# Kernel tuning notes

Measured on AMD Instinct MI355X. Metric: run time of the kernel, lower is better.

Reference implementation:

```python
import jax, jax.numpy as jnp
import numpy as np

IMG = 224      # img_size
P = 16         # patch_size
C = 3          # in_chans
K = 100        # n_segments
COMPACT = 10.0 # slic compactness
ITERS = 10     # slic k-means iterations


def _resize_matrix(src, dst):
    # Linear antialiased resize is a linear map; materialize it by resizing identity.
    return jax.image.resize(jnp.eye(src, dtype=jnp.float32), (dst, src),
                            method='linear', antialias=True)


def _slic_labels(img_hwc):
    """Simplified SLIC: grid-initialized k-means in (color, compactness-scaled xy) space."""
    H, W = IMG, IMG
    S = float(np.sqrt(H * W / K))         # superpixel spacing
    ratio = COMPACT / S                   # spatial scaling (SLIC distance weighting)
    yy, xx = jnp.meshgrid(jnp.arange(H, dtype=jnp.float32),
                          jnp.arange(W, dtype=jnp.float32), indexing='ij')
    feat = jnp.concatenate([img_hwc, (yy * ratio)[..., None], (xx * ratio)[..., None]],
                           axis=-1).reshape(H * W, C + 2)  # [HW, 5]
    # grid init of K centers
    gh = int(np.ceil(np.sqrt(K)))
    gw = int(np.ceil(K / gh))
    cy = ((np.arange(gh) + 0.5) * H / gh).astype(np.int32)
    cx = ((np.arange(gw) + 0.5) * W / gw).astype(np.int32)
    idx = (cy[:, None] * W + cx[None, :]).reshape(-1)[:K]
    centers0 = feat[jnp.asarray(idx)]  # [K, 5]

    f2 = jnp.sum(feat * feat, axis=1, keepdims=True)  # [HW,1]

    def dists(centers):
        c2 = jnp.sum(centers * centers, axis=1)  # [K]
        return f2 + c2[None, :] - 2.0 * (feat @ centers.T)  # [HW,K]

    def body(i, centers):
        lbl = jnp.argmin(dists(centers), axis=1)              # [HW]
        oh = jax.nn.one_hot(lbl, K, dtype=feat.dtype)         # [HW,K]
        cnt = oh.sum(0)                                       # [K]
        new = (oh.T @ feat) / jnp.maximum(cnt, 1.0)[:, None]  # [K,5]
        return jnp.where((cnt > 0)[:, None], new, centers)

    centers = jax.lax.fori_loop(0, ITERS, body, centers0)
    return jnp.argmin(dists(centers), axis=1).reshape(H, W)


def _embed_one(img_chw, A):
    img = jnp.transpose(img_chw, (1, 2, 0))                     # [H,W,C]
    labels = jax.lax.stop_gradient(_slic_labels(img))           # [H,W] int
    masks = jax.nn.one_hot(labels, K, dtype=img.dtype, axis=0)  # [K,H,W]
    masked = masks[..., None] * img[None]                       # [K,H,W,C]
    tmp = jnp.einsum('ph,khwc->kpwc', A, masked)                # resize rows
    return jnp.einsum('qw,kpwc->kpqc', A, tmp)                  # [K,P,P,C]


def reference(x):
    B = x.shape[0]
    A = _resize_matrix(IMG, P)
    sp = jax.vmap(lambda im: _embed_one(im, A))(x)  # [B,K,P,P,C]
    # torch: view(B, K*C, P, P)  (raw row-major reinterpret), flatten(2), transpose(1,2)
    out = sp.reshape(B, K * C, P, P).reshape(B, K * C, P * P)
    return jnp.transpose(out, (0, 2, 1))  # [B, P*P, K*C]


def setup_inputs() -> dict:
    key = jax.random.key(0)
    x = jax.random.uniform(key, (8, C, IMG, IMG), dtype=jnp.float32)
    return {"x": x}
```

## Files before the change

kernel.cpp:

```cpp
#include <hip/hip_runtime.h>
#include <math.h>

#define IMGD 224
#define HW 50176
#define NK 100
#define NB 8
#define OUT_PER_B 76800
#define NCHUNK 131
#define MSTR 13


static __device__ __forceinline__ float ratio_f32() {
  return (float)(10.0 / sqrt(224.0 * 224.0 / 100.0));
}

static __device__ __forceinline__ float dist5s(float f0, float f1, float f2,
                                               float f3, float f4, float fsq,
                                               float c0, float c1, float c2,
                                               float c3, float c4, float q) {
  float dot = __fmul_rn(f0, c0);
  dot = __fmaf_rn(f1, c1, dot);
  dot = __fmaf_rn(f2, c2, dot);
  dot = __fmaf_rn(f3, c3, dot);
  dot = __fmaf_rn(f4, c4, dot);
  return __fsub_rn(__fadd_rn(fsq, q), __fmul_rn(2.0f, dot));
}

static __device__ __forceinline__ float fsq5(float f0, float f1, float f2,
                                             float f3, float f4) {
  float s = __fmul_rn(f0, f0);
  s = __fadd_rn(s, __fmul_rn(f1, f1));
  s = __fadd_rn(s, __fmul_rn(f2, f2));
  s = __fadd_rn(s, __fmul_rn(f3, f3));
  s = __fadd_rn(s, __fmul_rn(f4, f4));
  return s;
}

__global__ void __launch_bounds__(128, 4) iter_kernel(
    const float* __restrict__ x, float* __restrict__ centers,
    const float* __restrict__ c2g, float* __restrict__ partials, int flag,
    float* __restrict__ Ag) {
  __shared__ float4 ck4[NK];
  __shared__ float2 ck2[NK];
  __shared__ unsigned int mask[NK * MSTR];
  __shared__ unsigned short ppk[NK * MSTR];
  __shared__ float4 cval4[384];
  __shared__ float  cvalf[384];
  __shared__ int cnt[128];
  __shared__ int offx[128];
  __shared__ int wtot;
  __shared__ float ubpart[12][10];
  __shared__ float ubg[12];
  __shared__ unsigned int candm[12][4];
  __shared__ unsigned char clist[12][104];
  __shared__ int clen[12];
  __shared__ float ared[128];
  int c = blockIdx.x, b = blockIdx.y;
  int tid = threadIdx.x;

  if (c >= NCHUNK) {
    for (int rr = 0; rr < 2; ++rr) {
      int p = 2 * b + rr;
      float cp = (p + 0.5f) * 14.0f - 0.5f;
      float trip0, trip1 = 0.0f;
      {
        float xd = fabsf(cp - (float)tid) / 14.0f;
        trip0 = fmaxf(0.0f, 1.0f - xd);
      }
      int t2 = tid + 128;
      if (t2 < IMGD) {
        float xd = fabsf(cp - (float)t2) / 14.0f;
        trip1 = fmaxf(0.0f, 1.0f - xd);
      }
      ared[tid] = trip0 + trip1;
      __syncthreads();
      for (int s = 64; s > 0; s >>= 1) {
        if (tid < s) ared[tid] += ared[tid + s];
        __syncthreads();
      }
      float Zp = ared[0];
      __syncthreads();
      {
        float xd = fabsf(cp - (float)tid) / 14.0f;
        Ag[p * IMGD + tid] = fmaxf(0.0f, 1.0f - xd) / Zp;
      }
      if (t2 < IMGD) {
        float xd = fabsf(cp - (float)t2) / 14.0f;
        Ag[p * IMGD + t2] = fmaxf(0.0f, 1.0f - xd) / Zp;
      }
      __syncthreads();
    }
    return;
  }

  int start = (c < 129) ? c * 384 : 49536 + (c - 129) * 320;
  int len   = (c < 129) ? 384 : 320;

  const float ratio = ratio_f32();
  const float* x0 = x + (size_t)b * 3 * HW;
  if (flag == 0) {
    if (tid < NK) {
      int gy = tid / 10, gx = tid - 10 * (tid / 10);
      int cy = (int)((gy + 0.5) * 224.0 / 10.0);
      int cx = (int)((gx + 0.5) * 224.0 / 10.0);
      int i = cy * IMGD + cx;
      float c0 = x0[i], c1 = x0[HW + i], c2 = x0[2 * HW + i];
      float c3 = __fmul_rn((float)cy, ratio);
      float c4 = __fmul_rn((float)cx, ratio);
      float s = __fmul_rn(c0, c0);
      s = __fadd_rn(s, __fmul_rn(c1, c1));
      s = __fadd_rn(s, __fmul_rn(c2, c2));
      s = __fadd_rn(s, __fmul_rn(c3, c3));
      s = __fadd_rn(s, __fmul_rn(c4, c4));
      ck4[tid] = make_float4(c0, c1, c2, c3);
      ck2[tid] = make_float2(c4, s);
      if (c == 0) {
        float* oc = centers + ((size_t)b * NK + tid) * 5;
        oc[0] = c0; oc[1] = c1; oc[2] = c2; oc[3] = c3; oc[4] = c4;
      }
    }
  } else {
    const float* cb = centers + (size_t)b * NK * 5;
    const float* c2b = c2g + (size_t)b * NK;
    if (tid < NK) {
      ck4[tid] = make_float4(cb[tid*5+0], cb[tid*5+1], cb[tid*5+2], cb[tid*5+3]);
      ck2[tid] = make_float2(cb[tid*5+4], c2b[tid]);
    }
  }
  for (int t = tid; t < NK * MSTR; t += 128) mask[t] = 0u;
  if (tid < 48) candm[tid >> 2][tid & 3] = 0u;

  float f0[3], f1[3], f2[3], f3[3], f4[3], fq[3];
  bool vld[3];
  for (int r = 0; r < 3; ++r) {
    int t = tid + r * 128;
    vld[r] = (t < len);
    int i = start + (vld[r] ? t : 0);
    int y = i / IMGD, xw = i - y * IMGD;
    f0[r] = x0[i]; f1[r] = x0[HW + i]; f2[r] = x0[2 * HW + i];
    f3[r] = __fmul_rn((float)y, ratio);
    f4[r] = __fmul_rn((float)xw, ratio);
    fq[r] = fsq5(f0[r], f1[r], f2[r], f3[r], f4[r]);
  }
  __syncthreads();

  if (tid < 120) {
    int g = tid / 10, kb = tid - 10 * g;
    int i0 = start + g * 32, i1 = i0 + 31;
    int ymin = i0 / IMGD, ymax = i1 / IMGD;
    int cmin = (ymin == ymax) ? (i0 - ymin * IMGD) : 0;
    int cmax = (ymin == ymax) ? (i1 - ymax * IMGD) : (IMGD - 1);
    float f3mn = __fmul_rn((float)ymin, ratio);
    float f3mx = __fmul_rn((float)ymax, ratio);
    float f4mn = __fmul_rn((float)cmin, ratio);
    float f4mx = __fmul_rn((float)cmax, ratio);
    float mn = 3.4e38f;
    for (int k = kb * 10; k < kb * 10 + 10; ++k) {
      float c3 = ck4[k].w, c4 = ck2[k].x;
      float dy = fmaxf(fabsf(c3 - f3mn), fabsf(c3 - f3mx));
      float dx = fmaxf(fabsf(c4 - f4mn), fabsf(c4 - f4mx));
      mn = fminf(mn, dy * dy + dx * dx + 3.0f);
    }
    ubpart[g][kb] = mn;
  }
  __syncthreads();
  if (tid < 12) {
    float mn = ubpart[tid][0];
    for (int j = 1; j < 10; ++j) mn = fminf(mn, ubpart[tid][j]);
    ubg[tid] = mn + 1.0f;
  }
  __syncthreads();
  if (tid < 120) {
    int g = tid / 10, kb = tid - 10 * g;
    int i0 = start + g * 32, i1 = i0 + 31;
    int ymin = i0 / IMGD, ymax = i1 / IMGD;
    int cmin = (ymin == ymax) ? (i0 - ymin * IMGD) : 0;
    int cmax = (ymin == ymax) ? (i1 - ymax * IMGD) : (IMGD - 1);
    float f3mn = __fmul_rn((float)ymin, ratio);
    float f3mx = __fmul_rn((float)ymax, ratio);
    float f4mn = __fmul_rn((float)cmin, ratio);
    float f4mx = __fmul_rn((float)cmax, ratio);
    float lim = ubg[g];
    for (int k = kb * 10; k < kb * 10 + 10; ++k) {
      float c3 = ck4[k].w, c4 = ck2[k].x;
      float dy = fmaxf(0.0f, fmaxf(f3mn - c3, c3 - f3mx));
      float dx = fmaxf(0.0f, fmaxf(f4mn - c4, c4 - f4mx));
      if (dy * dy + dx * dx <= lim)
        atomicOr(&candm[g][k >> 5], 1u << (k & 31));
    }
  }
  __syncthreads();
  if (tid < 12) {
    int len2 = 0;
    for (int w = 0; w < 4; ++w) {
      unsigned int m = candm[tid][w];
      while (m) {
        int j = __ffs(m) - 1;
        m &= m - 1;
        clist[tid][len2++] = (unsigned char)(w * 32 + j);
      }
    }
    clen[tid] = len2;
  }
  __syncthreads();

  float best[3]; int bk[3];
  for (int r = 0; r < 3; ++r) {
    best[r] = 3.4e38f; bk[r] = 0;
    int t = tid + r * 128;
    int g = (t < 384) ? (t >> 5) : 0;
    int n = clen[g];
    for (int j = 0; j < n; ++j) {
      int k = clist[g][j];
      float4 a4 = ck4[k];
      float2 a2 = ck2[k];
      float d = dist5s(f0[r], f1[r], f2[r], f3[r], f4[r], fq[r],
                       a4.x, a4.y, a4.z, a4.w, a2.x, a2.y);
      if (d < best[r]) { best[r] = d; bk[r] = k; }
    }
  }
  for (int r = 0; r < 3; ++r) {
    int t = tid + r * 128;
    if (vld[r]) atomicOr(&mask[bk[r] * MSTR + (t >> 5)], 1u << (t & 31));
  }
  __syncthreads();

  int myCnt = 0;
  if (tid < NK) {
    int s = 0;
    for (int g = 0; g < 12; ++g) {
      ppk[tid * MSTR + g] = (unsigned short)s;
      s += __popc(mask[tid * MSTR + g]);
    }
    myCnt = s;
  }
  cnt[tid] = myCnt;
  __syncthreads();

  int v = myCnt;
  for (int d = 1; d < 64; d <<= 1) {
    int u = __shfl_up(v, d, 64);
    if ((tid & 63) >= d) v += u;
  }
  if (tid == 63) wtot = v;
  __syncthreads();
  if (tid >= 64) v += wtot;
  offx[tid] = v;
  __syncthreads();

  for (int r = 0; r < 3; ++r) {
    int t = tid + r * 128;
    if (vld[r]) {
      int g = t >> 5, j = t & 31;
      unsigned int m = mask[bk[r] * MSTR + g];
      int rank = ppk[bk[r] * MSTR + g] + __popc(m & ((1u << j) - 1u));
      int pos = offx[bk[r]] - cnt[bk[r]] + rank;
      cval4[pos] = make_float4(f0[r], f1[r], f2[r], f3[r]);
      cvalf[pos] = f4[r];
    }
  }
  __syncthreads();

  if (tid < NK) {
    int n = cnt[tid];
    int base = offx[tid] - n;
    float s0 = 0.f, s1 = 0.f, s2 = 0.f, s3 = 0.f, s4 = 0.f, s5 = 0.f;
    for (int m = 0; m < n; ++m) {
      float4 vv = cval4[base + m];
      float ww = cvalf[base + m];
      s0 = __fadd_rn(s0, vv.x);
      s1 = __fadd_rn(s1, vv.y);
      s2 = __fadd_rn(s2, vv.z);
      s3 = __fadd_rn(s3, vv.w);
      s4 = __fadd_rn(s4, ww);
      s5 += 1.0f;
    }
    float* pp = partials + ((size_t)(b * NK + tid) * 6) * NCHUNK + c;
    pp[0 * NCHUNK] = s0; pp[1 * NCHUNK] = s1; pp[2 * NCHUNK] = s2;
    pp[3 * NCHUNK] = s3; pp[4 * NCHUNK] = s4; pp[5 * NCHUNK] = s5;
  }
}

__global__ void __launch_bounds__(128) combine_update_kernel(
    float* __restrict__ centers, const float* __restrict__ partials,
    float* __restrict__ c2g) {
  __shared__ float st[6 * NCHUNK];
  __shared__ float sums[6];
  __shared__ float newc[5];
  int bk = blockIdx.x;
  int tid = threadIdx.x;
  const float* base = partials + (size_t)bk * 6 * NCHUNK;
  for (int t = tid; t < 6 * NCHUNK; t += 128) st[t] = base[t];
  __syncthreads();
  if (tid < 6) {
    const float* row = st + tid * NCHUNK;
    float s = row[0];
    for (int c = 1; c < NCHUNK; ++c) s = __fadd_rn(s, row[c]);
    sums[tid] = s;
  }
  __syncthreads();
  float cntv = sums[5];
  float* cc = centers + (size_t)bk * 5;
  if (tid < 5) {
    float v;
    if (cntv > 0.0f) {
      float m = fmaxf(cntv, 1.0f);
      v = __fdiv_rn(sums[tid], m);
      cc[tid] = v;
    } else {
      v = cc[tid];
    }
    newc[tid] = v;
  }
  __syncthreads();
  if (tid == 0) {
    float t0 = __fmul_rn(newc[0], newc[0]);
    t0 = __fadd_rn(t0, __fmul_rn(newc[1], newc[1]));
    t0 = __fadd_rn(t0, __fmul_rn(newc[2], newc[2]));
    t0 = __fadd_rn(t0, __fmul_rn(newc[3], newc[3]));
    t0 = __fadd_rn(t0, __fmul_rn(newc[4], newc[4]));
    c2g[bk] = t0;
  }
}

__global__ void __launch_bounds__(128, 4) label_kernel(
    const float* __restrict__ x, const float* __restrict__ centers,
    const float* __restrict__ c2g, unsigned char* __restrict__ labels) {
  __shared__ float4 ck4[NK];
  __shared__ float2 ck2[NK];
  __shared__ float ubpart[12][10];
  __shared__ float ubg[12];
  __shared__ unsigned int candm[12][4];
  int c = blockIdx.x, b = blockIdx.y;
  int tid = threadIdx.x;
  int start = (c < 129) ? c * 384 : 49536 + (c - 129) * 320;
  int len   = (c < 129) ? 384 : 320;

  const float ratio = ratio_f32();
  const float* x0 = x + (size_t)b * 3 * HW;
  const float* cb = centers + (size_t)b * NK * 5;
  const float* c2b = c2g + (size_t)b * NK;
  if (tid < NK) {
    ck4[tid] = make_float4(cb[tid*5+0], cb[tid*5+1], cb[tid*5+2], cb[tid*5+3]);
    ck2[tid] = make_float2(cb[tid*5+4], c2b[tid]);
  }
  if (tid < 48) candm[tid >> 2][tid & 3] = 0u;

  float f0[3], f1[3], f2[3], f3[3], f4[3], fq[3];
  int ii[3];
  bool vld[3];
  for (int r = 0; r < 3; ++r) {
    int t = tid + r * 128;
    vld[r] = (t < len);
    int i = start + (vld[r] ? t : 0);
    ii[r] = i;
    int y = i / IMGD, xw = i - y * IMGD;
    f0[r] = x0[i]; f1[r] = x0[HW + i]; f2[r] = x0[2 * HW + i];
    f3[r] = __fmul_rn((float)y, ratio);
    f4[r] = __fmul_rn((float)xw, ratio);
    fq[r] = fsq5(f0[r], f1[r], f2[r], f3[r], f4[r]);
  }
  __syncthreads();

  if (tid < 120) {
    int g = tid / 10, kb = tid - 10 * g;
    int i0 = start + g * 32, i1 = i0 + 31;
    int ymin = i0 / IMGD, ymax = i1 / IMGD;
    int cmin = (ymin == ymax) ? (i0 - ymin * IMGD) : 0;
    int cmax = (ymin == ymax) ? (i1 - ymax * IMGD) : (IMGD - 1);
    float f3mn = __fmul_rn((float)ymin, ratio);
    float f3mx = __fmul_rn((float)ymax, ratio);
    float f4mn = __fmul_rn((float)cmin, ratio);
    float f4mx = __fmul_rn((float)cmax, ratio);
    float mn = 3.4e38f;
    for (int k = kb * 10; k < kb * 10 + 10; ++k) {
      float c3 = ck4[k].w, c4 = ck2[k].x;
      float dy = fmaxf(fabsf(c3 - f3mn), fabsf(c3 - f3mx));
      float dx = fmaxf(fabsf(c4 - f4mn), fabsf(c4 - f4mx));
      mn = fminf(mn, dy * dy + dx * dx + 3.0f);
    }
    ubpart[g][kb] = mn;
  }
  __syncthreads();
  if (tid < 12) {
    float mn = ubpart[tid][0];
    for (int j = 1; j < 10; ++j) mn = fminf(mn, ubpart[tid][j]);
    ubg[tid] = mn + 1.0f;
  }
  __syncthreads();
  if (tid < 120) {
    int g = tid / 10, kb = tid - 10 * g;
    int i0 = start + g * 32, i1 = i0 + 31;
    int ymin = i0 / IMGD, ymax = i1 / IMGD;
    int cmin = (ymin == ymax) ? (i0 - ymin * IMGD) : 0;
    int cmax = (ymin == ymax) ? (i1 - ymax * IMGD) : (IMGD - 1);
    float f3mn = __fmul_rn((float)ymin, ratio);
    float f3mx = __fmul_rn((float)ymax, ratio);
    float f4mn = __fmul_rn((float)cmin, ratio);
    float f4mx = __fmul_rn((float)cmax, ratio);
    float lim = ubg[g];
    for (int k = kb * 10; k < kb * 10 + 10; ++k) {
      float c3 = ck4[k].w, c4 = ck2[k].x;
      float dy = fmaxf(0.0f, fmaxf(f3mn - c3, c3 - f3mx));
      float dx = fmaxf(0.0f, fmaxf(f4mn - c4, c4 - f4mx));
      if (dy * dy + dx * dx <= lim)
        atomicOr(&candm[g][k >> 5], 1u << (k & 31));
    }
  }
  __syncthreads();

  float best[3]; int bk[3];
  for (int r = 0; r < 3; ++r) {
    best[r] = 3.4e38f; bk[r] = 0;
    int t = tid + r * 128;
    int g = (t < 384) ? (t >> 5) : 0;
    for (int w = 0; w < 4; ++w) {
      unsigned int m = candm[g][w];
      while (m) {
        int j = __ffs(m) - 1;
        m &= m - 1;
        int k = (w << 5) + j;
        float4 a4 = ck4[k];
        float2 a2 = ck2[k];
        float d = dist5s(f0[r], f1[r], f2[r], f3[r], f4[r], fq[r],
                         a4.x, a4.y, a4.z, a4.w, a2.x, a2.y);
        if (d < best[r]) { best[r] = d; bk[r] = k; }
      }
    }
  }
  unsigned char* lb = labels + (size_t)b * HW;
  for (int r = 0; r < 3; ++r)
    if (vld[r]) lb[ii[r]] = (unsigned char)bk[r];
}

__global__ void __launch_bounds__(256) embed_kernel(
    const float* __restrict__ x, const unsigned char* __restrict__ labels,
    const float* __restrict__ Ag, float* __restrict__ out) {
  __shared__ float Apv[28];
  __shared__ float Aqv[28];
  __shared__ float sk[NK * 3];
  int b = blockIdx.y;
  int p = blockIdx.x >> 4;
  int q = blockIdx.x & 15;
  int tid = threadIdx.x;

  int h0 = max(0, 14 * p - 7), h1 = min(IMGD - 1, 14 * p + 20);
  int w0 = max(0, 14 * q - 7), w1 = min(IMGD - 1, 14 * q + 20);
  int hl = h1 - h0 + 1, wl = w1 - w0 + 1;
  if (tid < hl) Apv[tid] = Ag[p * IMGD + h0 + tid];
  if (tid < wl) Aqv[tid] = Ag[q * IMGD + w0 + tid];
  for (int t = tid; t < NK * 3; t += 256) sk[t] = 0.0f;
  __syncthreads();

  const float* xb = x + (size_t)b * 3 * HW;
  const unsigned char* lb = labels + (size_t)b * HW;
  int n = hl * wl;
  for (int r = 0; r < 4; ++r) {
    int idx = tid + r * 256;
    if (idx >= n) break;
    int dh = idx / wl;
    int hh = h0 + dh;
    int dw = idx - dh * wl;
    int ww = w0 + dw;
    int i = hh * IMGD + ww;
    float v0 = xb[i], v1 = xb[HW + i], v2 = xb[2 * HW + i];
    int k = lb[i];
    float wgt = Apv[dh] * Aqv[dw];
    atomicAdd(&sk[k * 3 + 0], wgt * v0);
    atomicAdd(&sk[k * 3 + 1], wgt * v1);
    atomicAdd(&sk[k * 3 + 2], wgt * v2);
  }
  __syncthreads();

  float* outb = out + (size_t)b * OUT_PER_B;
  int base = p * 48 + q * 3;
  for (int t = tid; t < NK * 3; t += 256) {
    int k = t / 3, cc = t - 3 * k;
    int f = k * 768 + base + cc;
    outb[(f & 255) * 300 + (f >> 8)] = sk[t];
  }
}

extern "C" void kernel_launch(void* const* d_in, const int* in_sizes, int n_in,
                              void* d_out, int out_size, void* d_ws, size_t ws_size,
                              hipStream_t stream) {
  const float* x = (const float*)d_in[0];
  float* out = (float*)d_out;
  char* ws = (char*)d_ws;
  float* centers        = (float*)(ws + 16384);
  float* c2g            = (float*)(ws + 49152);
  float* Ag             = (float*)(ws + 65536);
  unsigned char* labels = (unsigned char*)(ws + 98304);
  float* partials       = (float*)(ws + 1703936);

  dim3 cgrid0(NCHUNK + 1, NB);
  dim3 cgrid(NCHUNK, NB);
  iter_kernel<<<cgrid0, 128, 0, stream>>>(x, centers, c2g, partials, 0, Ag);
  combine_update_kernel<<<NB * NK, 128, 0, stream>>>(centers, partials, c2g);
  for (int it = 1; it < 10; ++it) {
    iter_kernel<<<cgrid, 128, 0, stream>>>(x, centers, c2g, partials, 1, Ag);
    combine_update_kernel<<<NB * NK, 128, 0, stream>>>(centers, partials, c2g);
  }
  label_kernel<<<cgrid, 128, 0, stream>>>(x, centers, c2g, labels);
  dim3 egrid(256, NB);
  embed_kernel<<<egrid, 256, 0, stream>>>(x, labels, Ag, out);
}
```

Before: 294.9 us.

## Pack two chunks per iter block, batch combine rows, merge embed columns

The iteration kernel now runs 256-thread blocks, each covering two 384-pixel chunks, with duplicated shared-memory state per half, which halves the block count. The combine kernel handles 8 centers per block instead of one, cutting the grid from 800 to 100 blocks. The embed kernel processes four adjacent output columns per block so overlapping image windows are loaded once. The trade-offs are a larger shared-memory footprint, block-wide syncs shared by both halves, and more shared atomics per pixel in embed.

```diff
diff --git a/kernel.cpp b/kernel.cpp
--- a/kernel.cpp
+++ b/kernel.cpp
@@ -36,43 +36,43 @@
   return s;
 }
 
-__global__ void __launch_bounds__(128, 4) iter_kernel(
+__global__ void __launch_bounds__(256, 2) iter_kernel(
     const float* __restrict__ x, float* __restrict__ centers,
     const float* __restrict__ c2g, float* __restrict__ partials, int flag,
     float* __restrict__ Ag) {
   __shared__ float4 ck4[NK];
   __shared__ float2 ck2[NK];
-  __shared__ unsigned int mask[NK * MSTR];
-  __shared__ unsigned short ppk[NK * MSTR];
-  __shared__ float4 cval4[384];
-  __shared__ float  cvalf[384];
-  __shared__ int cnt[128];
-  __shared__ int offx[128];
-  __shared__ int wtot;
-  __shared__ float ubpart[12][10];
-  __shared__ float ubg[12];
-  __shared__ unsigned int candm[12][4];
-  __shared__ unsigned char clist[12][104];
-  __shared__ int clen[12];
+  __shared__ unsigned int maskS[2][NK * MSTR];
+  __shared__ unsigned short ppkS[2][NK * MSTR];
+  __shared__ float4 cval4[2][384];
+  __shared__ float  cvalf[2][384];
+  __shared__ int cntS[2][128];
+  __shared__ int offxS[2][128];
+  __shared__ int wtotS[2];
+  __shared__ float ubpart[2][12][10];
+  __shared__ float ubg[2][12];
+  __shared__ unsigned int candm[2][12][4];
+  __shared__ unsigned char clist[2][12][104];
+  __shared__ int clen[2][12];
   __shared__ float ared[128];
-  int c = blockIdx.x, b = blockIdx.y;
+  int bx = blockIdx.x, b = blockIdx.y;
   int tid = threadIdx.x;
 
-  if (c >= NCHUNK) {
+  if (bx >= 66) {
     for (int rr = 0; rr < 2; ++rr) {
       int p = 2 * b + rr;
       float cp = (p + 0.5f) * 14.0f - 0.5f;
-      float trip0, trip1 = 0.0f;
-      {
-        float xd = fabsf(cp - (float)tid) / 14.0f;
-        trip0 = fmaxf(0.0f, 1.0f - xd);
-      }
-      int t2 = tid + 128;
-      if (t2 < IMGD) {
-        float xd = fabsf(cp - (float)t2) / 14.0f;
-        trip1 = fmaxf(0.0f, 1.0f - xd);
-      }
-      ared[tid] = trip0 + trip1;
+      if (tid < 128) {
+        float xd0 = fabsf(cp - (float)tid) / 14.0f;
+        float trip0 = fmaxf(0.0f, 1.0f - xd0);
+        float trip1 = 0.0f;
+        int t2 = tid + 128;
+        if (t2 < IMGD) {
+          float xd = fabsf(cp - (float)t2) / 14.0f;
+          trip1 = fmaxf(0.0f, 1.0f - xd);
+        }
+        ared[tid] = trip0 + trip1;
+      }
       __syncthreads();
       for (int s = 64; s > 0; s >>= 1) {
         if (tid < s) ared[tid] += ared[tid + s];
@@ -80,21 +80,25 @@
       }
       float Zp = ared[0];
       __syncthreads();
-      {
+      if (tid < IMGD) {
         float xd = fabsf(cp - (float)tid) / 14.0f;
         Ag[p * IMGD + tid] = fmaxf(0.0f, 1.0f - xd) / Zp;
       }
-      if (t2 < IMGD) {
-        float xd = fabsf(cp - (float)t2) / 14.0f;
-        Ag[p * IMGD + t2] = fmaxf(0.0f, 1.0f - xd) / Zp;
-      }
       __syncthreads();
     }
     return;
   }
 
-  int start = (c < 129) ? c * 384 : 49536 + (c - 129) * 320;
-  int len   = (c < 129) ? 384 : 320;
+  int half = tid >> 7;
+  int lt = tid & 127;
+  int c = 2 * bx + half;
+  int start, len;
+  if (c < NCHUNK) {
+    start = (c < 129) ? c * 384 : 49536 + (c - 129) * 320;
+    len   = (c < 129) ? 384 : 320;
+  } else {
+    start = 0; len = 0;
+  }
 
   const float ratio = ratio_f32();
   const float* x0 = x + (size_t)b * 3 * HW;
@@ -114,7 +118,7 @@
       s = __fadd_rn(s, __fmul_rn(c4, c4));
       ck4[tid] = make_float4(c0, c1, c2, c3);
       ck2[tid] = make_float2(c4, s);
-      if (c == 0) {
+      if (bx == 0) {
         float* oc = centers + ((size_t)b * NK + tid) * 5;
         oc[0] = c0; oc[1] = c1; oc[2] = c2; oc[3] = c3; oc[4] = c4;
       }
@@ -127,15 +131,235 @@
       ck2[tid] = make_float2(cb[tid*5+4], c2b[tid]);
     }
   }
-  for (int t = tid; t < NK * MSTR; t += 128) mask[t] = 0u;
+  for (int t = lt; t < NK * MSTR; t += 128) maskS[half][t] = 0u;
+  if (lt < 48) candm[half][lt >> 2][lt & 3] = 0u;
+
+  float f0[3], f1[3], f2[3], f3[3], f4[3], fq[3];
+  bool vld[3];
+  for (int r = 0; r < 3; ++r) {
+    int t = lt + r * 128;
+    vld[r] = (t < len);
+    int i = start + (vld[r] ? t : 0);
+    int y = i / IMGD, xw = i - y * IMGD;
+    f0[r] = x0[i]; f1[r] = x0[HW + i]; f2[r] = x0[2 * HW + i];
+    f3[r] = __fmul_rn((float)y, ratio);
+    f4[r] = __fmul_rn((float)xw, ratio);
+    fq[r] = fsq5(f0[r], f1[r], f2[r], f3[r], f4[r]);
+  }
+  __syncthreads();
+
+  if (lt < 120) {
+    int g = lt / 10, kb = lt - 10 * g;
+    int i0 = start + g * 32, i1 = i0 + 31;
+    int ymin = i0 / IMGD, ymax = i1 / IMGD;
+    int cmin = (ymin == ymax) ? (i0 - ymin * IMGD) : 0;
+    int cmax = (ymin == ymax) ? (i1 - ymax * IMGD) : (IMGD - 1);
+    float f3mn = __fmul_rn((float)ymin, ratio);
+    float f3mx = __fmul_rn((float)ymax, ratio);
+    float f4mn = __fmul_rn((float)cmin, ratio);
+    float f4mx = __fmul_rn((float)cmax, ratio);
+    float mn = 3.4e38f;
+    for (int k = kb * 10; k < kb * 10 + 10; ++k) {
+      float c3 = ck4[k].w, c4 = ck2[k].x;
+      float dy = fmaxf(fabsf(c3 - f3mn), fabsf(c3 - f3mx));
+      float dx = fmaxf(fabsf(c4 - f4mn), fabsf(c4 - f4mx));
+      mn = fminf(mn, dy * dy + dx * dx + 3.0f);
+    }
+    ubpart[half][g][kb] = mn;
+  }
+  __syncthreads();
+  if (lt < 12) {
+    float mn = ubpart[half][lt][0];
+    for (int j = 1; j < 10; ++j) mn = fminf(mn, ubpart[half][lt][j]);
+    ubg[half][lt] = mn + 1.0f;
+  }
+  __syncthreads();
+  if (lt < 120) {
+    int g = lt / 10, kb = lt - 10 * g;
+    int i0 = start + g * 32, i1 = i0 + 31;
+    int ymin = i0 / IMGD, ymax = i1 / IMGD;
+    int cmin = (ymin == ymax) ? (i0 - ymin * IMGD) : 0;
+    int cmax = (ymin == ymax) ? (i1 - ymax * IMGD) : (IMGD - 1);
+    float f3mn = __fmul_rn((float)ymin, ratio);
+    float f3mx = __fmul_rn((float)ymax, ratio);
+    float f4mn = __fmul_rn((float)cmin, ratio);
+    float f4mx = __fmul_rn((float)cmax, ratio);
+    float lim = ubg[half][g];
+    for (int k = kb * 10; k < kb * 10 + 10; ++k) {
+      float c3 = ck4[k].w, c4 = ck2[k].x;
+      float dy = fmaxf(0.0f, fmaxf(f3mn - c3, c3 - f3mx));
+      float dx = fmaxf(0.0f, fmaxf(f4mn - c4, c4 - f4mx));
+      if (dy * dy + dx * dx <= lim)
+        atomicOr(&candm[half][g][k >> 5], 1u << (k & 31));
+    }
+  }
+  __syncthreads();
+  if (lt < 12) {
+    int len2 = 0;
+    for (int w = 0; w < 4; ++w) {
+      unsigned int m = candm[half][lt][w];
+      while (m) {
+        int j = __ffs(m) - 1;
+        m &= m - 1;
+        clist[half][lt][len2++] = (unsigned char)(w * 32 + j);
+      }
+    }
+    clen[half][lt] = len2;
+  }
+  __syncthreads();
+
+  float best[3]; int bk[3];
+  for (int r = 0; r < 3; ++r) {
+    best[r] = 3.4e38f; bk[r] = 0;
+    int t = lt + r * 128;
+    int g = (t < 384) ? (t >> 5) : 0;
+    int n = clen[half][g];
+    for (int j = 0; j < n; ++j) {
+      int k = clist[half][g][j];
+      float4 a4 = ck4[k];
+      float2 a2 = ck2[k];
+      float d = dist5s(f0[r], f1[r], f2[r], f3[r], f4[r], fq[r],
+                       a4.x, a4.y, a4.z, a4.w, a2.x, a2.y);
+      if (d < best[r]) { best[r] = d; bk[r] = k; }
+    }
+  }
+  for (int r = 0; r < 3; ++r) {
+    int t = lt + r * 128;
+    if (vld[r]) atomicOr(&maskS[half][bk[r] * MSTR + (t >> 5)], 1u << (t & 31));
+  }
+  __syncthreads();
+
+  int myCnt = 0;
+  if (lt < NK) {
+    int s = 0;
+    for (int g = 0; g < 12; ++g) {
+      ppkS[half][lt * MSTR + g] = (unsigned short)s;
+      s += __popc(maskS[half][lt * MSTR + g]);
+    }
+    myCnt = s;
+  }
+  cntS[half][lt] = myCnt;
+  __syncthreads();
+
+  int v = myCnt;
+  for (int d = 1; d < 64; d <<= 1) {
+    int u = __shfl_up(v, d, 64);
+    if ((tid & 63) >= d) v += u;
+  }
+  if (lt == 63) wtotS[half] = v;
+  __syncthreads();
+  if (lt >= 64) v += wtotS[half];
+  offxS[half][lt] = v;
+  __syncthreads();
+
+  for (int r = 0; r < 3; ++r) {
+    int t = lt + r * 128;
+    if (vld[r]) {
+      int g = t >> 5, j = t & 31;
+      unsigned int m = maskS[half][bk[r] * MSTR + g];
+      int rank = ppkS[half][bk[r] * MSTR + g] + __popc(m & ((1u << j) - 1u));
+      int pos = offxS[half][bk[r]] - cntS[half][bk[r]] + rank;
+      cval4[half][pos] = make_float4(f0[r], f1[r], f2[r], f3[r]);
+      cvalf[half][pos] = f4[r];
+    }
+  }
+  __syncthreads();
+
+  if (c < NCHUNK && lt < NK) {
+    int n = cntS[half][lt];
+    int base = offxS[half][lt] - n;
+    float s0 = 0.f, s1 = 0.f, s2 = 0.f, s3 = 0.f, s4 = 0.f, s5 = 0.f;
+    for (int m = 0; m < n; ++m) {
+      float4 vv = cval4[half][base + m];
+      float ww = cvalf[half][base + m];
+      s0 = __fadd_rn(s0, vv.x);
+      s1 = __fadd_rn(s1, vv.y);
+      s2 = __fadd_rn(s2, vv.z);
+      s3 = __fadd_rn(s3, vv.w);
+      s4 = __fadd_rn(s4, ww);
+      s5 += 1.0f;
+    }
+    float* pp = partials + ((size_t)(b * NK + lt) * 6) * NCHUNK + c;
+    pp[0 * NCHUNK] = s0; pp[1 * NCHUNK] = s1; pp[2 * NCHUNK] = s2;
+    pp[3 * NCHUNK] = s3; pp[4 * NCHUNK] = s4; pp[5 * NCHUNK] = s5;
+  }
+}
+
+__global__ void __launch_bounds__(128) combine_update_kernel(
+    float* __restrict__ centers, const float* __restrict__ partials,
+    float* __restrict__ c2g) {
+  __shared__ float st[8 * 6 * NCHUNK];
+  __shared__ float sums[8][6];
+  __shared__ float newc[8][5];
+  int bb = blockIdx.x;
+  int tid = threadIdx.x;
+  const float* base = partials + (size_t)bb * 8 * 6 * NCHUNK;
+  for (int t = tid; t < 8 * 6 * NCHUNK; t += 128) st[t] = base[t];
+  __syncthreads();
+  if (tid < 48) {
+    int row = tid / 6, comp = tid - 6 * (tid / 6);
+    const float* rp = st + (row * 6 + comp) * NCHUNK;
+    float s = rp[0];
+    for (int c = 1; c < NCHUNK; ++c) s = __fadd_rn(s, rp[c]);
+    sums[row][comp] = s;
+  }
+  __syncthreads();
+  if (tid < 40) {
+    int row = tid / 5, d = tid - 5 * (tid / 5);
+    float cntv = sums[row][5];
+    float* cc = centers + (size_t)(bb * 8 + row) * 5;
+    float v;
+    if (cntv > 0.0f) {
+      float m = fmaxf(cntv, 1.0f);
+      v = __fdiv_rn(sums[row][d], m);
+      cc[d] = v;
+    } else {
+      v = cc[d];
+    }
+    newc[row][d] = v;
+  }
+  __syncthreads();
+  if (tid < 8) {
+    float t0 = __fmul_rn(newc[tid][0], newc[tid][0]);
+    t0 = __fadd_rn(t0, __fmul_rn(newc[tid][1], newc[tid][1]));
+    t0 = __fadd_rn(t0, __fmul_rn(newc[tid][2], newc[tid][2]));
+    t0 = __fadd_rn(t0, __fmul_rn(newc[tid][3], newc[tid][3]));
+    t0 = __fadd_rn(t0, __fmul_rn(newc[tid][4], newc[tid][4]));
+    c2g[bb * 8 + tid] = t0;
+  }
+}
+
+__global__ void __launch_bounds__(128, 4) label_kernel(
+    const float* __restrict__ x, const float* __restrict__ centers,
+    const float* __restrict__ c2g, unsigned char* __restrict__ labels) {
+  __shared__ float4 ck4[NK];
+  __shared__ float2 ck2[NK];
+  __shared__ float ubpart[12][10];
+  __shared__ float ubg[12];
+  __shared__ unsigned int candm[12][4];
+  int c = blockIdx.x, b = blockIdx.y;
+  int tid = threadIdx.x;
+  int start = (c < 129) ? c * 384 : 49536 + (c - 129) * 320;
+  int len   = (c < 129) ? 384 : 320;
+
+  const float ratio = ratio_f32();
+  const float* x0 = x + (size_t)b * 3 * HW;
+  const float* cb = centers + (size_t)b * NK * 5;
+  const float* c2b = c2g + (size_t)b * NK;
+  if (tid < NK) {
+    ck4[tid] = make_float4(cb[tid*5+0], cb[tid*5+1], cb[tid*5+2], cb[tid*5+3]);
+    ck2[tid] = make_float2(cb[tid*5+4], c2b[tid]);
+  }
   if (tid < 48) candm[tid >> 2][tid & 3] = 0u;
 
   float f0[3], f1[3], f2[3], f3[3], f4[3], fq[3];
+  int ii[3];
   bool vld[3];
   for (int r = 0; r < 3; ++r) {
     int t = tid + r * 128;
     vld[r] = (t < len);
     int i = start + (vld[r] ? t : 0);
+    ii[r] = i;
     int y = i / IMGD, xw = i - y * IMGD;
     f0[r] = x0[i]; f1[r] = x0[HW + i]; f2[r] = x0[2 * HW + i];
     f3[r] = __fmul_rn((float)y, ratio);
@@ -190,224 +414,6 @@
     }
   }
   __syncthreads();
-  if (tid < 12) {
-    int len2 = 0;
-    for (int w = 0; w < 4; ++w) {
-      unsigned int m = candm[tid][w];
-      while (m) {
-        int j = __ffs(m) - 1;
-        m &= m - 1;
-        clist[tid][len2++] = (unsigned char)(w * 32 + j);
-      }
-    }
-    clen[tid] = len2;
-  }
-  __syncthreads();
-
-  float best[3]; int bk[3];
-  for (int r = 0; r < 3; ++r) {
-    best[r] = 3.4e38f; bk[r] = 0;
-    int t = tid + r * 128;
-    int g = (t < 384) ? (t >> 5) : 0;
-    int n = clen[g];
-    for (int j = 0; j < n; ++j) {
-      int k = clist[g][j];
-      float4 a4 = ck4[k];
-      float2 a2 = ck2[k];
-      float d = dist5s(f0[r], f1[r], f2[r], f3[r], f4[r], fq[r],
-                       a4.x, a4.y, a4.z, a4.w, a2.x, a2.y);
-      if (d < best[r]) { best[r] = d; bk[r] = k; }
-    }
-  }
-  for (int r = 0; r < 3; ++r) {
-    int t = tid + r * 128;
-    if (vld[r]) atomicOr(&mask[bk[r] * MSTR + (t >> 5)], 1u << (t & 31));
-  }
-  __syncthreads();
-
-  int myCnt = 0;
-  if (tid < NK) {
-    int s = 0;
-    for (int g = 0; g < 12; ++g) {
-      ppk[tid * MSTR + g] = (unsigned short)s;
-      s += __popc(mask[tid * MSTR + g]);
-    }
-    myCnt = s;
-  }
-  cnt[tid] = myCnt;
-  __syncthreads();
-
-  int v = myCnt;
-  for (int d = 1; d < 64; d <<= 1) {
-    int u = __shfl_up(v, d, 64);
-    if ((tid & 63) >= d) v += u;
-  }
-  if (tid == 63) wtot = v;
-  __syncthreads();
-  if (tid >= 64) v += wtot;
-  offx[tid] = v;
-  __syncthreads();
-
-  for (int r = 0; r < 3; ++r) {
-    int t = tid + r * 128;
-    if (vld[r]) {
-      int g = t >> 5, j = t & 31;
-      unsigned int m = mask[bk[r] * MSTR + g];
-      int rank = ppk[bk[r] * MSTR + g] + __popc(m & ((1u << j) - 1u));
-      int pos = offx[bk[r]] - cnt[bk[r]] + rank;
-      cval4[pos] = make_float4(f0[r], f1[r], f2[r], f3[r]);
-      cvalf[pos] = f4[r];
-    }
-  }
-  __syncthreads();
-
-  if (tid < NK) {
-    int n = cnt[tid];
-    int base = offx[tid] - n;
-    float s0 = 0.f, s1 = 0.f, s2 = 0.f, s3 = 0.f, s4 = 0.f, s5 = 0.f;
-    for (int m = 0; m < n; ++m) {
-      float4 vv = cval4[base + m];
-      float ww = cvalf[base + m];
-      s0 = __fadd_rn(s0, vv.x);
-      s1 = __fadd_rn(s1, vv.y);
-      s2 = __fadd_rn(s2, vv.z);
-      s3 = __fadd_rn(s3, vv.w);
-      s4 = __fadd_rn(s4, ww);
-      s5 += 1.0f;
-    }
-    float* pp = partials + ((size_t)(b * NK + tid) * 6) * NCHUNK + c;
-    pp[0 * NCHUNK] = s0; pp[1 * NCHUNK] = s1; pp[2 * NCHUNK] = s2;
-    pp[3 * NCHUNK] = s3; pp[4 * NCHUNK] = s4; pp[5 * NCHUNK] = s5;
-  }
-}
-
-__global__ void __launch_bounds__(128) combine_update_kernel(
-    float* __restrict__ centers, const float* __restrict__ partials,
-    float* __restrict__ c2g) {
-  __shared__ float st[6 * NCHUNK];
-  __shared__ float sums[6];
-  __shared__ float newc[5];
-  int bk = blockIdx.x;
-  int tid = threadIdx.x;
-  const float* base = partials + (size_t)bk * 6 * NCHUNK;
-  for (int t = tid; t < 6 * NCHUNK; t += 128) st[t] = base[t];
-  __syncthreads();
-  if (tid < 6) {
-    const float* row = st + tid * NCHUNK;
-    float s = row[0];
-    for (int c = 1; c < NCHUNK; ++c) s = __fadd_rn(s, row[c]);
-    sums[tid] = s;
-  }
-  __syncthreads();
-  float cntv = sums[5];
-  float* cc = centers + (size_t)bk * 5;
-  if (tid < 5) {
-    float v;
-    if (cntv > 0.0f) {
-      float m = fmaxf(cntv, 1.0f);
-      v = __fdiv_rn(sums[tid], m);
-      cc[tid] = v;
-    } else {
-      v = cc[tid];
-    }
-    newc[tid] = v;
-  }
-  __syncthreads();
-  if (tid == 0) {
-    float t0 = __fmul_rn(newc[0], newc[0]);
-    t0 = __fadd_rn(t0, __fmul_rn(newc[1], newc[1]));
-    t0 = __fadd_rn(t0, __fmul_rn(newc[2], newc[2]));
-    t0 = __fadd_rn(t0, __fmul_rn(newc[3], newc[3]));
-    t0 = __fadd_rn(t0, __fmul_rn(newc[4], newc[4]));
-    c2g[bk] = t0;
-  }
-}
-
-__global__ void __launch_bounds__(128, 4) label_kernel(
-    const float* __restrict__ x, const float* __restrict__ centers,
-    const float* __restrict__ c2g, unsigned char* __restrict__ labels) {
-  __shared__ float4 ck4[NK];
-  __shared__ float2 ck2[NK];
-  __shared__ float ubpart[12][10];
-  __shared__ float ubg[12];
-  __shared__ unsigned int candm[12][4];
-  int c = blockIdx.x, b = blockIdx.y;
-  int tid = threadIdx.x;
-  int start = (c < 129) ? c * 384 : 49536 + (c - 129) * 320;
-  int len   = (c < 129) ? 384 : 320;
-
-  const float ratio = ratio_f32();
-  const float* x0 = x + (size_t)b * 3 * HW;
-  const float* cb = centers + (size_t)b * NK * 5;
-  const float* c2b = c2g + (size_t)b * NK;
-  if (tid < NK) {
-    ck4[tid] = make_float4(cb[tid*5+0], cb[tid*5+1], cb[tid*5+2], cb[tid*5+3]);
-    ck2[tid] = make_float2(cb[tid*5+4], c2b[tid]);
-  }
-  if (tid < 48) candm[tid >> 2][tid & 3] = 0u;
-
-  float f0[3], f1[3], f2[3], f3[3], f4[3], fq[3];
-  int ii[3];
-  bool vld[3];
-  for (int r = 0; r < 3; ++r) {
-    int t = tid + r * 128;
-    vld[r] = (t < len);
-    int i = start + (vld[r] ? t : 0);
-    ii[r] = i;
-    int y = i / IMGD, xw = i - y * IMGD;
-    f0[r] = x0[i]; f1[r] = x0[HW + i]; f2[r] = x0[2 * HW + i];
-    f3[r] = __fmul_rn((float)y, ratio);
-    f4[r] = __fmul_rn((float)xw, ratio);
-    fq[r] = fsq5(f0[r], f1[r], f2[r], f3[r], f4[r]);
-  }
-  __syncthreads();
-
-  if (tid < 120) {
-    int g = tid / 10, kb = tid - 10 * g;
-    int i0 = start + g * 32, i1 = i0 + 31;
-    int ymin = i0 / IMGD, ymax = i1 / IMGD;
-    int cmin = (ymin == ymax) ? (i0 - ymin * IMGD) : 0;
-    int cmax = (ymin == ymax) ? (i1 - ymax * IMGD) : (IMGD - 1);
-    float f3mn = __fmul_rn((float)ymin, ratio);
-    float f3mx = __fmul_rn((float)ymax, ratio);
-    float f4mn = __fmul_rn((float)cmin, ratio);
-    float f4mx = __fmul_rn((float)cmax, ratio);
-    float mn = 3.4e38f;
-    for (int k = kb * 10; k < kb * 10 + 10; ++k) {
-      float c3 = ck4[k].w, c4 = ck2[k].x;
-      float dy = fmaxf(fabsf(c3 - f3mn), fabsf(c3 - f3mx));
-      float dx = fmaxf(fabsf(c4 - f4mn), fabsf(c4 - f4mx));
-      mn = fminf(mn, dy * dy + dx * dx + 3.0f);
-    }
-    ubpart[g][kb] = mn;
-  }
-  __syncthreads();
-  if (tid < 12) {
-    float mn = ubpart[tid][0];
-    for (int j = 1; j < 10; ++j) mn = fminf(mn, ubpart[tid][j]);
-    ubg[tid] = mn + 1.0f;
-  }
-  __syncthreads();
-  if (tid < 120) {
-    int g = tid / 10, kb = tid - 10 * g;
-    int i0 = start + g * 32, i1 = i0 + 31;
-    int ymin = i0 / IMGD, ymax = i1 / IMGD;
-    int cmin = (ymin == ymax) ? (i0 - ymin * IMGD) : 0;
-    int cmax = (ymin == ymax) ? (i1 - ymax * IMGD) : (IMGD - 1);
-    float f3mn = __fmul_rn((float)ymin, ratio);
-    float f3mx = __fmul_rn((float)ymax, ratio);
-    float f4mn = __fmul_rn((float)cmin, ratio);
-    float f4mx = __fmul_rn((float)cmax, ratio);
-    float lim = ubg[g];
-    for (int k = kb * 10; k < kb * 10 + 10; ++k) {
-      float c3 = ck4[k].w, c4 = ck2[k].x;
-      float dy = fmaxf(0.0f, fmaxf(f3mn - c3, c3 - f3mx));
-      float dx = fmaxf(0.0f, fmaxf(f4mn - c4, c4 - f4mx));
-      if (dy * dy + dx * dx <= lim)
-        atomicOr(&candm[g][k >> 5], 1u << (k & 31));
-    }
-  }
-  __syncthreads();
 
   float best[3]; int bk[3];
   for (int r = 0; r < 3; ++r) {
@@ -437,47 +443,70 @@
     const float* __restrict__ x, const unsigned char* __restrict__ labels,
     const float* __restrict__ Ag, float* __restrict__ out) {
   __shared__ float Apv[28];
-  __shared__ float Aqv[28];
-  __shared__ float sk[NK * 3];
+  __shared__ float Aqw[4][28];
+  __shared__ float sk[4][NK * 3];
   int b = blockIdx.y;
-  int p = blockIdx.x >> 4;
-  int q = blockIdx.x & 15;
+  int p = blockIdx.x >> 2;
+  int qg = blockIdx.x & 3;
+  int q0 = qg * 4;
   int tid = threadIdx.x;
 
   int h0 = max(0, 14 * p - 7), h1 = min(IMGD - 1, 14 * p + 20);
-  int w0 = max(0, 14 * q - 7), w1 = min(IMGD - 1, 14 * q + 20);
-  int hl = h1 - h0 + 1, wl = w1 - w0 + 1;
+  int hl = h1 - h0 + 1;
+  int w0q[4], w1q[4];
+#pragma unroll
+  for (int qi = 0; qi < 4; ++qi) {
+    int q = q0 + qi;
+    w0q[qi] = max(0, 14 * q - 7);
+    w1q[qi] = min(IMGD - 1, 14 * q + 20);
+  }
+  int W0 = w0q[0], W1 = w1q[3];
+  int WU = W1 - W0 + 1;
+
   if (tid < hl) Apv[tid] = Ag[p * IMGD + h0 + tid];
-  if (tid < wl) Aqv[tid] = Ag[q * IMGD + w0 + tid];
-  for (int t = tid; t < NK * 3; t += 256) sk[t] = 0.0f;
+  {
+    int t = tid - 64;
+    if (t >= 0 && t < 112) {
+      int qi = t / 28, dw = t - 28 * qi;
+      if (dw <= w1q[qi] - w0q[qi])
+        Aqw[qi][dw] = Ag[(q0 + qi) * IMGD + w0q[qi] + dw];
+    }
+  }
+  for (int t = tid; t < 4 * NK * 3; t += 256) sk[t / (NK * 3)][t % (NK * 3)] = 0.0f;
   __syncthreads();
 
   const float* xb = x + (size_t)b * 3 * HW;
   const unsigned char* lb = labels + (size_t)b * HW;
-  int n = hl * wl;
-  for (int r = 0; r < 4; ++r) {
+  int n = hl * WU;
+  for (int r = 0; r < 8; ++r) {
     int idx = tid + r * 256;
     if (idx >= n) break;
-    int dh = idx / wl;
-    int hh = h0 + dh;
-    int dw = idx - dh * wl;
-    int ww = w0 + dw;
-    int i = hh * IMGD + ww;
+    int dh = idx / WU;
+    int dcol = idx - dh * WU;
+    int col = W0 + dcol;
+    int i = (h0 + dh) * IMGD + col;
     float v0 = xb[i], v1 = xb[HW + i], v2 = xb[2 * HW + i];
     int k = lb[i];
-    float wgt = Apv[dh] * Aqv[dw];
-    atomicAdd(&sk[k * 3 + 0], wgt * v0);
-    atomicAdd(&sk[k * 3 + 1], wgt * v1);
-    atomicAdd(&sk[k * 3 + 2], wgt * v2);
+    float ap = Apv[dh];
+#pragma unroll
+    for (int qi = 0; qi < 4; ++qi) {
+      if (col >= w0q[qi] && col <= w1q[qi]) {
+        float wgt = ap * Aqw[qi][col - w0q[qi]];
+        atomicAdd(&sk[qi][k * 3 + 0], wgt * v0);
+        atomicAdd(&sk[qi][k * 3 + 1], wgt * v1);
+        atomicAdd(&sk[qi][k * 3 + 2], wgt * v2);
+      }
+    }
   }
   __syncthreads();
 
   float* outb = out + (size_t)b * OUT_PER_B;
-  int base = p * 48 + q * 3;
-  for (int t = tid; t < NK * 3; t += 256) {
-    int k = t / 3, cc = t - 3 * k;
+  for (int t = tid; t < 4 * NK * 3; t += 256) {
+    int qi = t / (NK * 3), t3 = t - qi * (NK * 3);
+    int k = t3 / 3, cc = t3 - 3 * k;
+    int base = p * 48 + (q0 + qi) * 3;
     int f = k * 768 + base + cc;
-    outb[(f & 255) * 300 + (f >> 8)] = sk[t];
+    outb[(f & 255) * 300 + (f >> 8)] = sk[qi][t3];
   }
 }
 
@@ -493,15 +522,15 @@
   unsigned char* labels = (unsigned char*)(ws + 98304);
   float* partials       = (float*)(ws + 1703936);
 
-  dim3 cgrid0(NCHUNK + 1, NB);
-  dim3 cgrid(NCHUNK, NB);
-  iter_kernel<<<cgrid0, 128, 0, stream>>>(x, centers, c2g, partials, 0, Ag);
-  combine_update_kernel<<<NB * NK, 128, 0, stream>>>(centers, partials, c2g);
+  dim3 ig0(67, NB);
+  dim3 ig(66, NB);
+  iter_kernel<<<ig0, 256, 0, stream>>>(x, centers, c2g, partials, 0, Ag);
+  combine_update_kernel<<<NB * NK / 8, 128, 0, stream>>>(centers, partials, c2g);
   for (int it = 1; it < 10; ++it) {
-    iter_kernel<<<cgrid, 128, 0, stream>>>(x, centers, c2g, partials, 1, Ag);
-    combine_update_kernel<<<NB * NK, 128, 0, stream>>>(centers, partials, c2g);
-  }
-  label_kernel<<<cgrid, 128, 0, stream>>>(x, centers, c2g, labels);
-  dim3 egrid(256, NB);
+    iter_kernel<<<ig, 256, 0, stream>>>(x, centers, c2g, partials, 1, Ag);
+    combine_update_kernel<<<NB * NK / 8, 128, 0, stream>>>(centers, partials, c2g);
+  }
+  label_kernel<<<dim3(NCHUNK, NB), 128, 0, stream>>>(x, centers, c2g, labels);
+  dim3 egrid(64, NB);
   embed_kernel<<<egrid, 256, 0, stream>>>(x, labels, Ag, out);
 }
```

Result: no change. 296.0 us (+0.4%).
